# Performance work log

Hardware: AMD Instinct MI355X
Metric: run time of the kernel (lower is better)

The kernel has to match this reference:

```python
import jax, jax.numpy as jnp
import numpy as np

BATCH, IN_DIM, H, W = 16, 32, 128, 128
BASE_OUT = 32


def setup_inputs() -> dict:
    key = jax.random.key(0)
    k_x, k_w2, k_b2, k_w1, k_b1 = jax.random.split(key, 5)
    x = jax.random.normal(k_x, (BATCH, IN_DIM, H, W), dtype=jnp.float32)
    # Conv2d(input_dim, 4*base_out, 1): weight (4bo, in_dim) after squeezing 1x1 kernel
    s2 = 1.0 / np.sqrt(IN_DIM)
    W2 = jax.random.uniform(k_w2, (4 * BASE_OUT, IN_DIM), jnp.float32, -s2, s2)
    b2 = jax.random.uniform(k_b2, (4 * BASE_OUT,), jnp.float32, -s2, s2)
    # Conv1d(base_out, 4*base_out, 2): weight (4bo, bo, 2)
    s1 = 1.0 / np.sqrt(BASE_OUT * 2)
    W1 = jax.random.uniform(k_w1, (4 * BASE_OUT, BASE_OUT, 2), jnp.float32, -s1, s1)
    b1 = jax.random.uniform(k_b1, (4 * BASE_OUT,), jnp.float32, -s1, s1)
    return {"x": x, "W2": W2, "b2": b2, "W1": W1, "b1": b1}


def reference(x, W2, b2, W1, b1):
    b, c, h, w = x.shape
    bo = W1.shape[1]  # base_out
    # skew: row i of x is placed at columns [i, i+w) of a (h, 2w-1) canvas
    rows = jnp.arange(h)
    cols = rows[:, None] + jnp.arange(w)[None, :]  # (h, w)
    skewed = jnp.zeros((b, c, h, 2 * w - 1), x.dtype).at[:, :, rows[:, None], cols].set(x)
    # 1x1 conv over channels: input-to-state pre-activations
    i2s = jnp.einsum('oc,bchy->bohy', W2, skewed) + b2[None, :, None, None]
    # original loops only over the first w skewed columns
    xs = jnp.moveaxis(i2s[:, :, :, :w], 3, 0)  # (w, b, 4bo, h)
    W1_prev, W1_cur = W1[:, :, 0], W1[:, :, 1]

    def step(carry, xt):
        pc, ph = carry  # (b, bo, h) each
        # Conv1d(kernel=2) on [0, prev_h]: tap 0 sees ph shifted right by one
        ph_shift = jnp.pad(ph, ((0, 0), (0, 0), (1, 0)))[:, :, :-1]
        s2s = (jnp.einsum('oc,bch->boh', W1_prev, ph_shift)
               + jnp.einsum('oc,bch->boh', W1_cur, ph)
               + b1[None, :, None])
        g = xt + s2s
        o = jax.nn.sigmoid(g[:, 0 * bo:1 * bo])
        f = jax.nn.sigmoid(g[:, 1 * bo:2 * bo])
        i = jax.nn.sigmoid(g[:, 2 * bo:3 * bo])
        gg = jnp.tanh(g[:, 3 * bo:4 * bo])
        nc = f * pc + i * gg
        nh = o * jnp.tanh(nc)
        return (nc, nh), nh

    c0 = jnp.zeros((b, bo, h), x.dtype)
    _, hs = jax.lax.scan(step, (c0, c0), xs)  # hs: (w, b, bo, h)
    return jnp.moveaxis(hs, 0, -1)  # (b, bo, h, w)
```

## Files before the change

### kernel.cpp

```cpp
#include <hip/hip_runtime.h>
#include <stdint.h>

#define BATCH 16
#define CIN   32
#define HH    128
#define WW    128
#define BO    32
#define OCH   128
#define NCH   16
#define NW    8
#define DEPTH 64


__global__ __launch_bounds__(512, 2) void diag_lstm_scan(
    const float* __restrict__ x, const float* __restrict__ W2g,
    const float* __restrict__ b2, const float* __restrict__ W1g,
    const float* __restrict__ b1, float* __restrict__ out,
    int* __restrict__ progress, unsigned long long* __restrict__ hand)
{
    const int tid = threadIdx.x;
    const int l   = tid & 63;
    const int w   = tid >> 6;
    const int blk = blockIdx.x;
    const int b = (blk & 7) + ((blk >> 7) << 3);
    const int k = (blk >> 3) & (NCH - 1);
    const int row = k * NW + w;

    __shared__ __attribute__((aligned(16))) float phs[2][NW + 1][BO];
    __shared__ __attribute__((aligned(16))) float xbuf[NW][CIN];
    __shared__ __attribute__((aligned(16))) float gbuf[NW][OCH];

    for (int i = tid; i < 2 * (NW + 1) * BO; i += 512) ((float*)phs)[i] = 0.f;

    const int o0 = 2 * l, o1 = 2 * l + 1;
    float w2a[CIN], w2b[CIN], w1pa[CIN], w1ca[CIN], w1pb[CIN], w1cb[CIN];
#pragma unroll
    for (int c = 0; c < CIN; ++c) {
        w2a[c]  = W2g[o0 * CIN + c];
        w2b[c]  = W2g[o1 * CIN + c];
        w1pa[c] = W1g[(o0 * CIN + c) * 2 + 0];
        w1ca[c] = W1g[(o0 * CIN + c) * 2 + 1];
        w1pb[c] = W1g[(o1 * CIN + c) * 2 + 0];
        w1cb[c] = W1g[(o1 * CIN + c) * 2 + 1];
    }
    const float biasA = b2[o0] + b1[o0];
    const float biasB = b2[o1] + b1[o1];

    const int j = l & 31;
    float pc = 0.f, ob0 = 0.f, ob1 = 0.f, ob2 = 0.f;
    float* outrow = out + ((size_t)(b * BO + j) * HH + row) * WW;

    const int kprev = (k > 0) ? k - 1 : 0;
    const unsigned long long* srcbase =
        hand + (size_t)((b * NCH + kprev) * DEPTH) * BO + j;
    unsigned long long* dstbase =
        hand + (size_t)((b * NCH + k) * DEPTH) * BO + j;
    int* myprog   = progress + (b * NCH + k);
    int* consprog = progress + (b * NCH + k) + 1;

    unsigned long long pre = 0ull;

    __syncthreads();

    for (int t = 0; t < WW; ++t) {
        const int par = t & 1;

        if (l < 32) {
            const int wp = t - row;
            float v = (wp >= 0) ? x[((size_t)(b * CIN + l) * HH + row) * WW + wp] : 0.f;
            xbuf[w][l] = v;
        }
        if (w == 0 && k > 0) {
            if (t > 0) {
                unsigned long long q = pre;
                while (__any((unsigned)(q >> 32) != (unsigned)t)) {
                    q = __hip_atomic_load(&srcbase[(size_t)((t - 1) & (DEPTH - 1)) * BO],
                                          __ATOMIC_RELAXED, __HIP_MEMORY_SCOPE_AGENT);
                }
                if (l < 32) phs[par][0][l] = __uint_as_float((unsigned)q);
            }
            pre = __hip_atomic_load(&srcbase[(size_t)(t & (DEPTH - 1)) * BO],
                                    __ATOMIC_RELAXED, __HIP_MEMORY_SCOPE_AGENT);
        }
        asm volatile("s_waitcnt lgkmcnt(0)" ::: "memory");

        float ga = biasA, gb = biasB;
        {
            const float4* xb4 = (const float4*)(&xbuf[w][0]);
            const float4* pv4 = (const float4*)(&phs[par][w][0]);
            const float4* qv4 = (const float4*)(&phs[par][w + 1][0]);
#pragma unroll
            for (int cc = 0; cc < CIN / 4; ++cc) {
                const float4 xv = xb4[cc];
                const float4 pv = pv4[cc];
                const float4 qv = qv4[cc];
                const float* xs = (const float*)&xv;
                const float* ps = (const float*)&pv;
                const float* qs = (const float*)&qv;
#pragma unroll
                for (int ci = 0; ci < 4; ++ci) {
                    const int c = 4 * cc + ci;
                    ga = fmaf(w2a[c],  xs[ci], ga);
                    gb = fmaf(w2b[c],  xs[ci], gb);
                    ga = fmaf(w1pa[c], ps[ci], ga);
                    gb = fmaf(w1pb[c], ps[ci], gb);
                    ga = fmaf(w1ca[c], qs[ci], ga);
                    gb = fmaf(w1cb[c], qs[ci], gb);
                }
            }
        }
        *(float2*)&gbuf[w][o0] = make_float2(ga, gb);
        asm volatile("s_waitcnt lgkmcnt(0)" ::: "memory");

        if (l < 32) {
            if (w == NW - 1 && k < NCH - 1 && (t & 15) == 0 && t >= 48) {
                while (__hip_atomic_load(consprog, __ATOMIC_RELAXED,
                                         __HIP_MEMORY_SCOPE_AGENT) < t - 47) { }
            }
            const float go = gbuf[w][l];
            const float gf = gbuf[w][32 + l];
            const float gi = gbuf[w][64 + l];
            const float gg = gbuf[w][96 + l];
            const float so = 1.f / (1.f + __expf(-go));
            const float sf = 1.f / (1.f + __expf(-gf));
            const float si = 1.f / (1.f + __expf(-gi));
            const float tg = 2.f / (1.f + __expf(-2.f * gg)) - 1.f;
            const float nc = sf * pc + si * tg;
            const float th = 2.f / (1.f + __expf(-2.f * nc)) - 1.f;
            const float nh = so * th;
            pc = nc;
            phs[par ^ 1][w + 1][l] = nh;

            const int ph4 = t & 3;
            if (ph4 == 0) ob0 = nh;
            else if (ph4 == 1) ob1 = nh;
            else if (ph4 == 2) ob2 = nh;
            else *(float4*)(outrow + (t - 3)) = make_float4(ob0, ob1, ob2, nh);

            if (w == NW - 1 && k < NCH - 1) {
                unsigned long long q = ((unsigned long long)(unsigned)(t + 1) << 32)
                                     | (unsigned long long)__float_as_uint(nh);
                __hip_atomic_store(&dstbase[(size_t)(t & (DEPTH - 1)) * BO], q,
                                   __ATOMIC_RELAXED, __HIP_MEMORY_SCOPE_AGENT);
            }
            if (w == 0 && l == 0) {
                __hip_atomic_store(myprog, t + 1, __ATOMIC_RELAXED,
                                   __HIP_MEMORY_SCOPE_AGENT);
            }
        }
        __syncthreads();
    }
}

extern "C" void kernel_launch(void* const* d_in, const int* in_sizes, int n_in,
                              void* d_out, int out_size, void* d_ws, size_t ws_size,
                              hipStream_t stream) {
    const float* x  = (const float*)d_in[0];
    const float* W2 = (const float*)d_in[1];
    const float* b2 = (const float*)d_in[2];
    const float* W1 = (const float*)d_in[3];
    const float* b1 = (const float*)d_in[4];
    float* out = (float*)d_out;

    int* progress = (int*)d_ws;
    unsigned long long* hand = (unsigned long long*)((char*)d_ws + 4096);

    const size_t clr = 4096 + (size_t)BATCH * NCH * DEPTH * BO * 8;
    hipMemsetAsync(d_ws, 0, clr, stream);

    dim3 grid(BATCH * NCH), block(512);
    hipLaunchKernelGGL(diag_lstm_scan, grid, block, 0, stream,
                       x, W2, b2, W1, b1, out, progress, hand);
}
```

Baseline: 218.6 us.

## Precompute input-to-state projection before the recurrent scan and prefetch it per step

Before the serial scan, each block now computes the 1x1-conv input projection for its rows across all time steps and writes it to a workspace buffer (128 MB). Each step then prefetches one float2 of that projection instead of loading x and doing the W2 FMAs. This takes half the FMA work and the W2 registers off the latency-bound recurrent critical path. In exchange it adds a large global write and read-back and depends on enough workspace; if the workspace is too small, a fallback keeps the old kernel.

```diff
diff --git a/kernel.cpp b/kernel.cpp
--- a/kernel.cpp
+++ b/kernel.cpp
@@ -11,12 +11,15 @@
 #define NW    8
 #define DEPTH 64
 
-
-__global__ __launch_bounds__(512, 2) void diag_lstm_scan(
+#define RINGSZ ((size_t)BATCH * NCH * DEPTH * BO * 8)
+#define I2SSZ  ((size_t)BATCH * HH * WW * OCH * 4)
+
+__global__ __launch_bounds__(512, 2) void diag_lstm_scan_v5(
     const float* __restrict__ x, const float* __restrict__ W2g,
     const float* __restrict__ b2, const float* __restrict__ W1g,
     const float* __restrict__ b1, float* __restrict__ out,
-    int* __restrict__ progress, unsigned long long* __restrict__ hand)
+    int* __restrict__ progress, unsigned long long* __restrict__ hand,
+    float* __restrict__ i2s)
 {
     const int tid = threadIdx.x;
     const int l   = tid & 63;
@@ -27,24 +30,78 @@
     const int row = k * NW + w;
 
     __shared__ __attribute__((aligned(16))) float phs[2][NW + 1][BO];
-    __shared__ __attribute__((aligned(16))) float xbuf[NW][CIN];
+    __shared__ __attribute__((aligned(16))) float xtile[NW][CIN][32];
     __shared__ __attribute__((aligned(16))) float gbuf[NW][OCH];
 
     for (int i = tid; i < 2 * (NW + 1) * BO; i += 512) ((float*)phs)[i] = 0.f;
 
     const int o0 = 2 * l, o1 = 2 * l + 1;
-    float w2a[CIN], w2b[CIN], w1pa[CIN], w1ca[CIN], w1pb[CIN], w1cb[CIN];
+    float* myi2s = i2s + (size_t)(b * HH + row) * WW * OCH;
+
+    {
+        float w2a_[CIN], w2b_[CIN];
+#pragma unroll
+        for (int c = 0; c < CIN; ++c) {
+            w2a_[c] = W2g[o0 * CIN + c];
+            w2b_[c] = W2g[o1 * CIN + c];
+        }
+        const float biasA = b2[o0] + b1[o0];
+        const float biasB = b2[o1] + b1[o1];
+
+        for (int t0 = 0; t0 < WW; t0 += 32) {
+#pragma unroll
+            for (int it = 0; it < 16; ++it) {
+                const int idx = it * 64 + l;
+                const int c = idx >> 5, i = idx & 31;
+                const int wp = t0 + i - row;
+                xtile[w][c][i] = (wp >= 0)
+                    ? x[((size_t)(b * CIN + c) * HH + row) * WW + wp] : 0.f;
+            }
+            asm volatile("s_waitcnt lgkmcnt(0)" ::: "memory");
+
+            float accA[32], accB[32];
+#pragma unroll
+            for (int i = 0; i < 32; ++i) { accA[i] = biasA; accB[i] = biasB; }
+#pragma unroll
+            for (int c = 0; c < CIN; ++c) {
+                const float4* xq = (const float4*)&xtile[w][c][0];
+#pragma unroll
+                for (int q = 0; q < 8; ++q) {
+                    const float4 xv = xq[q];
+                    accA[4*q+0] = fmaf(w2a_[c], xv.x, accA[4*q+0]);
+                    accB[4*q+0] = fmaf(w2b_[c], xv.x, accB[4*q+0]);
+                    accA[4*q+1] = fmaf(w2a_[c], xv.y, accA[4*q+1]);
+                    accB[4*q+1] = fmaf(w2b_[c], xv.y, accB[4*q+1]);
+                    accA[4*q+2] = fmaf(w2a_[c], xv.z, accA[4*q+2]);
+                    accB[4*q+2] = fmaf(w2b_[c], xv.z, accB[4*q+2]);
+                    accA[4*q+3] = fmaf(w2a_[c], xv.w, accA[4*q+3]);
+                    accB[4*q+3] = fmaf(w2b_[c], xv.w, accB[4*q+3]);
+                }
+            }
+#pragma unroll
+            for (int i = 0; i < 32; ++i) {
+                *(float2*)&myi2s[(size_t)(t0 + i) * OCH + o0] =
+                    make_float2(accA[i], accB[i]);
+            }
+            __syncthreads();
+        }
+    }
+    asm volatile("s_waitcnt vmcnt(0)" ::: "memory");
+    __syncthreads();
+
+    float w1pa[CIN], w1ca[CIN], w1pb[CIN], w1cb[CIN];
 #pragma unroll
     for (int c = 0; c < CIN; ++c) {
-        w2a[c]  = W2g[o0 * CIN + c];
-        w2b[c]  = W2g[o1 * CIN + c];
         w1pa[c] = W1g[(o0 * CIN + c) * 2 + 0];
         w1ca[c] = W1g[(o0 * CIN + c) * 2 + 1];
         w1pb[c] = W1g[(o1 * CIN + c) * 2 + 0];
         w1cb[c] = W1g[(o1 * CIN + c) * 2 + 1];
     }
-    const float biasA = b2[o0] + b1[o0];
-    const float biasB = b2[o1] + b1[o1];
+#pragma unroll
+    for (int c = 0; c < CIN; ++c) {
+        asm volatile("" : "+v"(w1pa[c]), "+v"(w1ca[c]),
+                          "+v"(w1pb[c]), "+v"(w1cb[c]));
+    }
 
     const int j = l & 31;
     float pc = 0.f, ob0 = 0.f, ob1 = 0.f, ob2 = 0.f;
@@ -59,17 +116,18 @@
     int* consprog = progress + (b * NCH + k) + 1;
 
     unsigned long long pre = 0ull;
+    const float2* myi2s2 = (const float2*)myi2s;
+    float2 ipre = myi2s2[l];
 
     __syncthreads();
 
     for (int t = 0; t < WW; ++t) {
         const int par = t & 1;
 
-        if (l < 32) {
-            const int wp = t - row;
-            float v = (wp >= 0) ? x[((size_t)(b * CIN + l) * HH + row) * WW + wp] : 0.f;
-            xbuf[w][l] = v;
-        }
+        const float2 icur = ipre;
+        const int tn = (t + 1 < WW) ? t + 1 : WW - 1;
+        ipre = myi2s2[(size_t)tn * 64 + l];
+
         if (w == 0 && k > 0) {
             if (t > 0) {
                 unsigned long long q = pre;
@@ -84,24 +142,19 @@
         }
         asm volatile("s_waitcnt lgkmcnt(0)" ::: "memory");
 
-        float ga = biasA, gb = biasB;
+        float ga = icur.x, gb = icur.y;
         {
-            const float4* xb4 = (const float4*)(&xbuf[w][0]);
             const float4* pv4 = (const float4*)(&phs[par][w][0]);
             const float4* qv4 = (const float4*)(&phs[par][w + 1][0]);
 #pragma unroll
             for (int cc = 0; cc < CIN / 4; ++cc) {
-                const float4 xv = xb4[cc];
                 const float4 pv = pv4[cc];
                 const float4 qv = qv4[cc];
-                const float* xs = (const float*)&xv;
                 const float* ps = (const float*)&pv;
                 const float* qs = (const float*)&qv;
 #pragma unroll
                 for (int ci = 0; ci < 4; ++ci) {
                     const int c = 4 * cc + ci;
-                    ga = fmaf(w2a[c],  xs[ci], ga);
-                    gb = fmaf(w2b[c],  xs[ci], gb);
                     ga = fmaf(w1pa[c], ps[ci], ga);
                     gb = fmaf(w1pb[c], ps[ci], gb);
                     ga = fmaf(w1ca[c], qs[ci], ga);
@@ -152,6 +205,144 @@
     }
 }
 
+__global__ __launch_bounds__(512, 2) void diag_lstm_scan_v4(
+    const float* __restrict__ x, const float* __restrict__ W2g,
+    const float* __restrict__ b2, const float* __restrict__ W1g,
+    const float* __restrict__ b1, float* __restrict__ out,
+    int* __restrict__ progress, unsigned long long* __restrict__ hand)
+{
+    const int tid = threadIdx.x;
+    const int l   = tid & 63;
+    const int w   = tid >> 6;
+    const int blk = blockIdx.x;
+    const int b = (blk & 7) + ((blk >> 7) << 3);
+    const int k = (blk >> 3) & (NCH - 1);
+    const int row = k * NW + w;
+
+    __shared__ __attribute__((aligned(16))) float phs[2][NW + 1][BO];
+    __shared__ __attribute__((aligned(16))) float xbuf[NW][CIN];
+    __shared__ __attribute__((aligned(16))) float gbuf[NW][OCH];
+
+    for (int i = tid; i < 2 * (NW + 1) * BO; i += 512) ((float*)phs)[i] = 0.f;
+
+    const int o0 = 2 * l, o1 = 2 * l + 1;
+    float w2a[CIN], w2b[CIN], w1pa[CIN], w1ca[CIN], w1pb[CIN], w1cb[CIN];
+#pragma unroll
+    for (int c = 0; c < CIN; ++c) {
+        w2a[c]  = W2g[o0 * CIN + c];
+        w2b[c]  = W2g[o1 * CIN + c];
+        w1pa[c] = W1g[(o0 * CIN + c) * 2 + 0];
+        w1ca[c] = W1g[(o0 * CIN + c) * 2 + 1];
+        w1pb[c] = W1g[(o1 * CIN + c) * 2 + 0];
+        w1cb[c] = W1g[(o1 * CIN + c) * 2 + 1];
+    }
+    const float biasA = b2[o0] + b1[o0];
+    const float biasB = b2[o1] + b1[o1];
+
+    const int j = l & 31;
+    float pc = 0.f, ob0 = 0.f, ob1 = 0.f, ob2 = 0.f;
+    float* outrow = out + ((size_t)(b * BO + j) * HH + row) * WW;
+
+    const int kprev = (k > 0) ? k - 1 : 0;
+    const unsigned long long* srcbase =
+        hand + (size_t)((b * NCH + kprev) * DEPTH) * BO + j;
+    unsigned long long* dstbase =
+        hand + (size_t)((b * NCH + k) * DEPTH) * BO + j;
+    int* myprog   = progress + (b * NCH + k);
+    int* consprog = progress + (b * NCH + k) + 1;
+
+    unsigned long long pre = 0ull;
+    __syncthreads();
+
+    for (int t = 0; t < WW; ++t) {
+        const int par = t & 1;
+        if (l < 32) {
+            const int wp = t - row;
+            xbuf[w][l] = (wp >= 0)
+                ? x[((size_t)(b * CIN + l) * HH + row) * WW + wp] : 0.f;
+        }
+        if (w == 0 && k > 0) {
+            if (t > 0) {
+                unsigned long long q = pre;
+                while (__any((unsigned)(q >> 32) != (unsigned)t)) {
+                    q = __hip_atomic_load(&srcbase[(size_t)((t - 1) & (DEPTH - 1)) * BO],
+                                          __ATOMIC_RELAXED, __HIP_MEMORY_SCOPE_AGENT);
+                }
+                if (l < 32) phs[par][0][l] = __uint_as_float((unsigned)q);
+            }
+            pre = __hip_atomic_load(&srcbase[(size_t)(t & (DEPTH - 1)) * BO],
+                                    __ATOMIC_RELAXED, __HIP_MEMORY_SCOPE_AGENT);
+        }
+        asm volatile("s_waitcnt lgkmcnt(0)" ::: "memory");
+
+        float ga = biasA, gb = biasB;
+        {
+            const float4* xb4 = (const float4*)(&xbuf[w][0]);
+            const float4* pv4 = (const float4*)(&phs[par][w][0]);
+            const float4* qv4 = (const float4*)(&phs[par][w + 1][0]);
+#pragma unroll
+            for (int cc = 0; cc < CIN / 4; ++cc) {
+                const float4 xv = xb4[cc];
+                const float4 pv = pv4[cc];
+                const float4 qv = qv4[cc];
+                const float* xs = (const float*)&xv;
+                const float* ps = (const float*)&pv;
+                const float* qs = (const float*)&qv;
+#pragma unroll
+                for (int ci = 0; ci < 4; ++ci) {
+                    const int c = 4 * cc + ci;
+                    ga = fmaf(w2a[c],  xs[ci], ga);
+                    gb = fmaf(w2b[c],  xs[ci], gb);
+                    ga = fmaf(w1pa[c], ps[ci], ga);
+                    gb = fmaf(w1pb[c], ps[ci], gb);
+                    ga = fmaf(w1ca[c], qs[ci], ga);
+                    gb = fmaf(w1cb[c], qs[ci], gb);
+                }
+            }
+        }
+        *(float2*)&gbuf[w][o0] = make_float2(ga, gb);
+        asm volatile("s_waitcnt lgkmcnt(0)" ::: "memory");
+
+        if (l < 32) {
+            if (w == NW - 1 && k < NCH - 1 && (t & 15) == 0 && t >= 48) {
+                while (__hip_atomic_load(consprog, __ATOMIC_RELAXED,
+                                         __HIP_MEMORY_SCOPE_AGENT) < t - 47) { }
+            }
+            const float go = gbuf[w][l];
+            const float gf = gbuf[w][32 + l];
+            const float gi = gbuf[w][64 + l];
+            const float gg = gbuf[w][96 + l];
+            const float so = 1.f / (1.f + __expf(-go));
+            const float sf = 1.f / (1.f + __expf(-gf));
+            const float si = 1.f / (1.f + __expf(-gi));
+            const float tg = 2.f / (1.f + __expf(-2.f * gg)) - 1.f;
+            const float nc = sf * pc + si * tg;
+            const float th = 2.f / (1.f + __expf(-2.f * nc)) - 1.f;
+            const float nh = so * th;
+            pc = nc;
+            phs[par ^ 1][w + 1][l] = nh;
+
+            const int ph4 = t & 3;
+            if (ph4 == 0) ob0 = nh;
+            else if (ph4 == 1) ob1 = nh;
+            else if (ph4 == 2) ob2 = nh;
+            else *(float4*)(outrow + (t - 3)) = make_float4(ob0, ob1, ob2, nh);
+
+            if (w == NW - 1 && k < NCH - 1) {
+                unsigned long long q = ((unsigned long long)(unsigned)(t + 1) << 32)
+                                     | (unsigned long long)__float_as_uint(nh);
+                __hip_atomic_store(&dstbase[(size_t)(t & (DEPTH - 1)) * BO], q,
+                                   __ATOMIC_RELAXED, __HIP_MEMORY_SCOPE_AGENT);
+            }
+            if (w == 0 && l == 0) {
+                __hip_atomic_store(myprog, t + 1, __ATOMIC_RELAXED,
+                                   __HIP_MEMORY_SCOPE_AGENT);
+            }
+        }
+        __syncthreads();
+    }
+}
+
 extern "C" void kernel_launch(void* const* d_in, const int* in_sizes, int n_in,
                               void* d_out, int out_size, void* d_ws, size_t ws_size,
                               hipStream_t stream) {
@@ -164,11 +355,18 @@
 
     int* progress = (int*)d_ws;
     unsigned long long* hand = (unsigned long long*)((char*)d_ws + 4096);
-
-    const size_t clr = 4096 + (size_t)BATCH * NCH * DEPTH * BO * 8;
-    hipMemsetAsync(d_ws, 0, clr, stream);
+    float* i2s = (float*)((char*)d_ws + 4096 + RINGSZ);
+
+    const size_t need = 4096 + RINGSZ + I2SSZ;
+
+    hipMemsetAsync(d_ws, 0, 4096 + RINGSZ, stream);
 
     dim3 grid(BATCH * NCH), block(512);
-    hipLaunchKernelGGL(diag_lstm_scan, grid, block, 0, stream,
-                       x, W2, b2, W1, b1, out, progress, hand);
+    if (ws_size >= need) {
+        hipLaunchKernelGGL(diag_lstm_scan_v5, grid, block, 0, stream,
+                           x, W2, b2, W1, b1, out, progress, hand, i2s);
+    } else {
+        hipLaunchKernelGGL(diag_lstm_scan_v4, grid, block, 0, stream,
+                           x, W2, b2, W1, b1, out, progress, hand);
+    }
 }
```

Measured after the change: 263.8 us. 1.21x slower.

## Add MFMA fp16 fused LSTM scan kernel with 4 row-chunks per batch

Applied to the files above, without the earlier changes.

Adds a new kernel that computes the gate pre-activations for 32 rows per block using fp16 MFMA 16x16x32 instructions. The input projection and both Conv1d taps are folded into one interleaved K dimension. The number of chained chunks per batch drops from 16 to 4 (64 blocks of 256 threads), the next x column is prefetched into a double buffer, and __syncthreads is replaced by an LDS flag spin barrier. This is meant to shorten the per-step critical path and the cross-block handoff chain. The cost is fp16 precision on weights and hidden state and far fewer active CUs. The old kernel is kept as a fallback when the workspace is too small.

```diff
diff --git a/kernel.cpp b/kernel.cpp
--- a/kernel.cpp
+++ b/kernel.cpp
@@ -7,12 +7,178 @@
 #define WW    128
 #define BO    32
 #define OCH   128
-#define NCH   16
-#define NW    8
+#define NCH   4
+#define RPC   32
 #define DEPTH 64
 
-
-__global__ __launch_bounds__(512, 2) void diag_lstm_scan(
+#define RINGSZ ((size_t)BATCH * NCH * DEPTH * BO * 8)
+#define RINGV4 ((size_t)BATCH * 16 * DEPTH * BO * 8)
+
+typedef _Float16 f16x8v __attribute__((ext_vector_type(8)));
+typedef float    f32x4v __attribute__((ext_vector_type(4)));
+
+__global__ __launch_bounds__(256) void diag_lstm_fused_v15(
+    const float* __restrict__ x,  const float* __restrict__ W2g,
+    const float* __restrict__ b2, const float* __restrict__ W1g,
+    const float* __restrict__ b1, float* __restrict__ out,
+    int* __restrict__ progress, unsigned long long* __restrict__ hand)
+{
+    const int tid = threadIdx.x;
+    const int l   = tid & 63;
+    const int w   = tid >> 6;
+    const int m   = w >> 1;
+    const int p   = w & 1;
+    const int kq  = l >> 4;
+    const int col = l & 15;
+    const int blk = blockIdx.x;
+    const int b   = blk & 15;
+    const int k   = blk >> 4;
+
+    __shared__ _Float16 ILV[2][33][68];
+    __shared__ _Float16 W1s[OCH][72];
+    __shared__ _Float16 W2s[OCH][40];
+    __shared__ _Float16 xls[2][32][36];
+    __shared__ float    bsh[OCH];
+    __shared__ int      sc[4];
+
+    for (int i = tid; i < OCH * CIN; i += 256) {
+        const int o = i >> 5, c = i & 31;
+        const float2 wv = *(const float2*)&W1g[((size_t)o * CIN + c) * 2];
+        W1s[o][2 * c]     = (_Float16)wv.x;
+        W1s[o][2 * c + 1] = (_Float16)wv.y;
+        W2s[o][c]         = (_Float16)W2g[(size_t)o * CIN + c];
+    }
+    if (tid < OCH) bsh[tid] = b2[tid] + b1[tid];
+    for (int i = tid; i < 2 * 33 * 68; i += 256) (&ILV[0][0][0])[i] = (_Float16)0.f;
+    if (tid < 4) sc[tid] = 0;
+
+    const int sr  = tid >> 3;
+    const int sc4 = (tid & 7) * 4;
+    const int srow = k * RPC + sr;
+    {
+        const int wp = 0 - srow;
+#pragma unroll
+        for (int e = 0; e < 4; ++e)
+            xls[0][sr][sc4 + e] = (wp >= 0)
+                ? (_Float16)x[((size_t)(b * CIN + sc4 + e) * HH + srow) * WW + wp]
+                : (_Float16)0.f;
+    }
+
+    const int j     = 16 * p + col;
+    const int rl0   = 16 * m + 4 * kq;
+    const int grow0 = k * RPC + rl0;
+    float pc[4] = {0.f, 0.f, 0.f, 0.f};
+
+    const unsigned long long* srcring =
+        hand + ((size_t)(b * NCH + (k > 0 ? k - 1 : 0)) * DEPTH) * BO + l;
+    unsigned long long* dstring =
+        hand + ((size_t)(b * NCH + k) * DEPTH) * BO + j;
+    int* myprog   = progress + (b * NCH + k);
+    int* consprog = myprog + 1;
+    unsigned long long pre = 0ull;
+
+    __syncthreads();
+
+    for (int t = 0; t < WW; ++t) {
+        const int par = t & 1;
+        _Float16 (*PS)[68] = ILV[par];
+        _Float16 (*PD)[68] = ILV[par ^ 1];
+
+        if (w <= 1 && k > 0 && t > 0) {
+            unsigned long long qv = pre;
+            while (__any(l < 32 && (unsigned)(qv >> 32) != (unsigned)t)) {
+                if (l < 32)
+                    qv = __hip_atomic_load(&srcring[(size_t)((t - 1) & 63) * BO],
+                                           __ATOMIC_RELAXED, __HIP_MEMORY_SCOPE_AGENT);
+            }
+            if (l < 32) {
+                PS[0][2 * l] = (_Float16)__uint_as_float((unsigned)qv);
+                pre = __hip_atomic_load(&srcring[(size_t)(t & 63) * BO],
+                                        __ATOMIC_RELAXED, __HIP_MEMORY_SCOPE_AGENT);
+            }
+        }
+        asm volatile("s_waitcnt lgkmcnt(0)" ::: "memory");
+
+        const f16x8v af0 = *(const f16x8v*)&PS[16 * m + col][8 * kq];
+        const f16x8v af1 = *(const f16x8v*)&PS[16 * m + col][32 + 8 * kq];
+        const f16x8v af2 = *(const f16x8v*)&xls[par][16 * m + col][8 * kq];
+
+        {
+            const int tn = (t + 1 < WW) ? t + 1 : WW - 1;
+            const int wp = tn - srow;
+#pragma unroll
+            for (int e = 0; e < 4; ++e)
+                xls[par ^ 1][sr][sc4 + e] = (wp >= 0)
+                    ? (_Float16)x[((size_t)(b * CIN + sc4 + e) * HH + srow) * WW + wp]
+                    : (_Float16)0.f;
+        }
+
+        f32x4v acc[4];
+#pragma unroll
+        for (int s = 0; s < 4; ++s) {
+            const int o = (p + 2 * s) * 16 + col;
+            const float bv = bsh[o];
+            acc[s][0] = bv; acc[s][1] = bv; acc[s][2] = bv; acc[s][3] = bv;
+            const f16x8v bw2 = *(const f16x8v*)&W2s[o][8 * kq];
+            const f16x8v bw0 = *(const f16x8v*)&W1s[o][8 * kq];
+            const f16x8v bw1 = *(const f16x8v*)&W1s[o][32 + 8 * kq];
+            acc[s] = __builtin_amdgcn_mfma_f32_16x16x32_f16(af2, bw2, acc[s], 0, 0, 0);
+            acc[s] = __builtin_amdgcn_mfma_f32_16x16x32_f16(af0, bw0, acc[s], 0, 0, 0);
+            acc[s] = __builtin_amdgcn_mfma_f32_16x16x32_f16(af1, bw1, acc[s], 0, 0, 0);
+        }
+
+        if (m == 1 && k < NCH - 1 && l == 0 && (t & 15) == 0 && t >= 48) {
+            while (__hip_atomic_load(consprog, __ATOMIC_RELAXED,
+                                     __HIP_MEMORY_SCOPE_AGENT) < t - 39) { }
+        }
+
+#pragma unroll
+        for (int e = 0; e < 4; ++e) {
+            const float go = acc[0][e], gf = acc[1][e], gi = acc[2][e], gg = acc[3][e];
+            const float so = 1.f / (1.f + __expf(-go));
+            const float sf = 1.f / (1.f + __expf(-gf));
+            const float si = 1.f / (1.f + __expf(-gi));
+            const float tg = 2.f / (1.f + __expf(-2.f * gg)) - 1.f;
+            const float nc = sf * pc[e] + si * tg;
+            const float th = 2.f / (1.f + __expf(-2.f * nc)) - 1.f;
+            const float nh = so * th;
+            pc[e] = nc;
+            const int rl = rl0 + e;
+            PD[rl][2 * j + 1] = (_Float16)nh;
+            PD[rl + 1][2 * j] = (_Float16)nh;
+            out[((size_t)(b * BO + j) * HH + (grow0 + e)) * WW + t] = nh;
+            if (m == 1 && kq == 3 && e == 3 && k < NCH - 1) {
+                unsigned long long qq =
+                    ((unsigned long long)(unsigned)(t + 1) << 32)
+                  | (unsigned long long)__float_as_uint(nh);
+                __hip_atomic_store(&dstring[(size_t)(t & 63) * BO], qq,
+                                   __ATOMIC_RELAXED, __HIP_MEMORY_SCOPE_AGENT);
+            }
+        }
+        if (w == 0 && l == 0) {
+            __hip_atomic_store(myprog, t + 1, __ATOMIC_RELAXED,
+                               __HIP_MEMORY_SCOPE_AGENT);
+        }
+
+        asm volatile("s_waitcnt lgkmcnt(0)" ::: "memory");
+        if (l == 0)
+            __hip_atomic_store(&sc[w], t + 1, __ATOMIC_RELAXED,
+                               __HIP_MEMORY_SCOPE_WORKGROUP);
+        for (;;) {
+            const int v0 = __hip_atomic_load(&sc[0], __ATOMIC_RELAXED,
+                                             __HIP_MEMORY_SCOPE_WORKGROUP);
+            const int v1 = __hip_atomic_load(&sc[1], __ATOMIC_RELAXED,
+                                             __HIP_MEMORY_SCOPE_WORKGROUP);
+            const int v2 = __hip_atomic_load(&sc[2], __ATOMIC_RELAXED,
+                                             __HIP_MEMORY_SCOPE_WORKGROUP);
+            const int v3 = __hip_atomic_load(&sc[3], __ATOMIC_RELAXED,
+                                             __HIP_MEMORY_SCOPE_WORKGROUP);
+            if (v0 >= t + 1 && v1 >= t + 1 && v2 >= t + 1 && v3 >= t + 1) break;
+        }
+    }
+}
+
+__global__ __launch_bounds__(512, 2) void diag_lstm_scan_v4(
     const float* __restrict__ x, const float* __restrict__ W2g,
     const float* __restrict__ b2, const float* __restrict__ W1g,
     const float* __restrict__ b1, float* __restrict__ out,
@@ -23,14 +189,14 @@
     const int w   = tid >> 6;
     const int blk = blockIdx.x;
     const int b = (blk & 7) + ((blk >> 7) << 3);
-    const int k = (blk >> 3) & (NCH - 1);
-    const int row = k * NW + w;
-
-    __shared__ __attribute__((aligned(16))) float phs[2][NW + 1][BO];
-    __shared__ __attribute__((aligned(16))) float xbuf[NW][CIN];
-    __shared__ __attribute__((aligned(16))) float gbuf[NW][OCH];
-
-    for (int i = tid; i < 2 * (NW + 1) * BO; i += 512) ((float*)phs)[i] = 0.f;
+    const int k = (blk >> 3) & 15;
+    const int row = k * 8 + w;
+
+    __shared__ __attribute__((aligned(16))) float phs[2][9][BO];
+    __shared__ __attribute__((aligned(16))) float xbuf[8][CIN];
+    __shared__ __attribute__((aligned(16))) float gbuf2[8][OCH];
+
+    for (int i = tid; i < 2 * 9 * BO; i += 512) ((float*)phs)[i] = 0.f;
 
     const int o0 = 2 * l, o1 = 2 * l + 1;
     float w2a[CIN], w2b[CIN], w1pa[CIN], w1ca[CIN], w1pb[CIN], w1cb[CIN];
@@ -52,23 +218,21 @@
 
     const int kprev = (k > 0) ? k - 1 : 0;
     const unsigned long long* srcbase =
-        hand + (size_t)((b * NCH + kprev) * DEPTH) * BO + j;
+        hand + (size_t)((b * 16 + kprev) * DEPTH) * BO + j;
     unsigned long long* dstbase =
-        hand + (size_t)((b * NCH + k) * DEPTH) * BO + j;
-    int* myprog   = progress + (b * NCH + k);
-    int* consprog = progress + (b * NCH + k) + 1;
+        hand + (size_t)((b * 16 + k) * DEPTH) * BO + j;
+    int* myprog   = progress + (b * 16 + k);
+    int* consprog = myprog + 1;
 
     unsigned long long pre = 0ull;
-
     __syncthreads();
 
     for (int t = 0; t < WW; ++t) {
         const int par = t & 1;
-
         if (l < 32) {
             const int wp = t - row;
-            float v = (wp >= 0) ? x[((size_t)(b * CIN + l) * HH + row) * WW + wp] : 0.f;
-            xbuf[w][l] = v;
+            xbuf[w][l] = (wp >= 0)
+                ? x[((size_t)(b * CIN + l) * HH + row) * WW + wp] : 0.f;
         }
         if (w == 0 && k > 0) {
             if (t > 0) {
@@ -109,18 +273,18 @@
                 }
             }
         }
-        *(float2*)&gbuf[w][o0] = make_float2(ga, gb);
+        *(float2*)&gbuf2[w][o0] = make_float2(ga, gb);
         asm volatile("s_waitcnt lgkmcnt(0)" ::: "memory");
 
         if (l < 32) {
-            if (w == NW - 1 && k < NCH - 1 && (t & 15) == 0 && t >= 48) {
+            if (w == 7 && k < 15 && (t & 15) == 0 && t >= 48) {
                 while (__hip_atomic_load(consprog, __ATOMIC_RELAXED,
                                          __HIP_MEMORY_SCOPE_AGENT) < t - 47) { }
             }
-            const float go = gbuf[w][l];
-            const float gf = gbuf[w][32 + l];
-            const float gi = gbuf[w][64 + l];
-            const float gg = gbuf[w][96 + l];
+            const float go = gbuf2[w][l];
+            const float gf = gbuf2[w][32 + l];
+            const float gi = gbuf2[w][64 + l];
+            const float gg = gbuf2[w][96 + l];
             const float so = 1.f / (1.f + __expf(-go));
             const float sf = 1.f / (1.f + __expf(-gf));
             const float si = 1.f / (1.f + __expf(-gi));
@@ -129,7 +293,7 @@
             const float th = 2.f / (1.f + __expf(-2.f * nc)) - 1.f;
             const float nh = so * th;
             pc = nc;
-            phs[par ^ 1][w + 1][l] = nh;
+            phs[par ^ 1][w + 1][j] = nh;
 
             const int ph4 = t & 3;
             if (ph4 == 0) ob0 = nh;
@@ -137,7 +301,7 @@
             else if (ph4 == 2) ob2 = nh;
             else *(float4*)(outrow + (t - 3)) = make_float4(ob0, ob1, ob2, nh);
 
-            if (w == NW - 1 && k < NCH - 1) {
+            if (w == 7 && k < 15) {
                 unsigned long long q = ((unsigned long long)(unsigned)(t + 1) << 32)
                                      | (unsigned long long)__float_as_uint(nh);
                 __hip_atomic_store(&dstbase[(size_t)(t & (DEPTH - 1)) * BO], q,
@@ -165,10 +329,13 @@
     int* progress = (int*)d_ws;
     unsigned long long* hand = (unsigned long long*)((char*)d_ws + 4096);
 
-    const size_t clr = 4096 + (size_t)BATCH * NCH * DEPTH * BO * 8;
-    hipMemsetAsync(d_ws, 0, clr, stream);
-
-    dim3 grid(BATCH * NCH), block(512);
-    hipLaunchKernelGGL(diag_lstm_scan, grid, block, 0, stream,
-                       x, W2, b2, W1, b1, out, progress, hand);
+    if (ws_size >= 4096 + RINGSZ) {
+        hipMemsetAsync(d_ws, 0, 4096 + RINGSZ, stream);
+        hipLaunchKernelGGL(diag_lstm_fused_v15, dim3(BATCH * NCH), dim3(256), 0,
+                           stream, x, W2, b2, W1, b1, out, progress, hand);
+    } else {
+        hipMemsetAsync(d_ws, 0, 4096 + RINGV4, stream);
+        hipLaunchKernelGGL(diag_lstm_scan_v4, dim3(BATCH * 16), dim3(512), 0,
+                           stream, x, W2, b2, W1, b1, out, progress, hand);
+    }
 }
```

Result: slower. 290.2 us (+32.8%).
